# Optimization experiments

Measured on AMD Instinct MI355X. Metric: run time of the kernel, lower is better.

The kernel has to match this reference:

```python
import jax, jax.numpy as jnp
import numpy as np

D = 2048          # n_embd
H = 4 * D         # hidden_size
B, S = 4, 2048


def _make_masks(seed=0):
    rng = np.random.default_rng(seed)
    # mask1: for each group of 4 output rows, keep 2 of 4 rows (whole rows)
    mask1 = np.zeros((H, D), dtype=np.float32)
    for i in range(0, H, 4):
        keep = rng.permutation(4)[:2] + i
        mask1[keep, :] = 1.0
    # mask2: for each group of 4 input columns, keep 2 of 4 columns
    mask2 = np.zeros((D, H), dtype=np.float32)
    for i in range(0, H, 4):
        keep = rng.permutation(4)[:2] + i
        mask2[:, keep] = 1.0
    return jnp.asarray(mask1), jnp.asarray(mask2)


def setup_inputs() -> dict:
    key = jax.random.key(0)
    k_x, k_w1, k_w2 = jax.random.split(key, 3)
    x = jax.random.normal(k_x, (B, S, D), dtype=jnp.float32)
    # Kaiming-uniform-ish init like nn.Linear defaults
    w1 = jax.random.uniform(k_w1, (H, D), dtype=jnp.float32, minval=-1.0, maxval=1.0) / np.sqrt(D)
    w2 = jax.random.uniform(k_w2, (D, H), dtype=jnp.float32, minval=-1.0, maxval=1.0) / np.sqrt(H)
    mask1, mask2 = _make_masks()
    return {"x": x, "w1": w1, "w2": w2, "mask1": mask1, "mask2": mask2}


def reference(x, w1, w2, mask1, mask2):
    # sparse_multiply is elementwise mask application on the weights
    sw1 = w1 * mask1                      # [H, D]
    sw2 = w2 * mask2                      # [D, H]
    h = jnp.einsum('bsd,hd->bsh', x, sw1) # F.linear(x, sw1)
    h = jax.nn.gelu(h, approximate=False) # torch F.gelu default = exact erf
    out = jnp.einsum('bsh,dh->bsd', h, sw2)
    return out
```

## Files before the change

### kernel.cpp

```cpp
#include <hip/hip_runtime.h>
#include <hip/hip_bf16.h>

typedef __bf16 bf16_t;
typedef __bf16 bf16x8 __attribute__((ext_vector_type(8)));
typedef float f32x4 __attribute__((ext_vector_type(4)));

__device__ __forceinline__ unsigned short f32_to_bf16_rn(float f) {
  unsigned u = __float_as_uint(f);
  u += 0x7fffu + ((u >> 16) & 1u);
  return (unsigned short)(u >> 16);
}

__device__ __forceinline__ float gelu_exact(float x) {
  return 0.5f * x * (1.0f + erff(x * 0.7071067811865475f));
}

#define GLDS16(g, l)                                                          \
  __builtin_amdgcn_global_load_lds(                                           \
      (const __attribute__((address_space(1))) void*)(g),                     \
      (__attribute__((address_space(3))) void*)(l), 16, 0, 0)

__global__ void cast_x_kernel(const float* __restrict__ in,
                              unsigned short* __restrict__ out, int n4) {
  int i = blockIdx.x * blockDim.x + threadIdx.x;
  if (i >= n4) return;
  float4 v = ((const float4*)in)[i];
  ushort4 o;
  o.x = f32_to_bf16_rn(v.x);
  o.y = f32_to_bf16_rn(v.y);
  o.z = f32_to_bf16_rn(v.z);
  o.w = f32_to_bf16_rn(v.w);
  ((ushort4*)out)[i] = o;
}

__global__ void build_idx_kernel(const float* __restrict__ mask1,
                                 const float* __restrict__ mask2,
                                 int* __restrict__ idx, int* __restrict__ meta,
                                 int H, int D) {
  __shared__ int sums[1024];
  const int t = threadIdx.x;
  int flags[8];
  int tot = 0;
#pragma unroll
  for (int u = 0; u < 8; ++u) {
    int j = t * 8 + u;
    int f = (mask1[(long long)j * D] != 0.0f) && (mask2[j] != 0.0f);
    flags[u] = f;
    tot += f;
  }
  sums[t] = tot;
  __syncthreads();
  for (int off = 1; off < 1024; off <<= 1) {
    int v = (t >= off) ? sums[t - off] : 0;
    __syncthreads();
    sums[t] += v;
    __syncthreads();
  }
  int pos = sums[t] - tot;
#pragma unroll
  for (int u = 0; u < 8; ++u) {
    if (flags[u]) idx[pos++] = t * 8 + u;
  }
  if (t == 1023) {
    int count = sums[1023];
    meta[0] = count;
    meta[1] = (count + 127) & ~127;
  }
}

__global__ void compact_w1_kernel(const float* __restrict__ w1,
                                  const int* __restrict__ idx,
                                  const int* __restrict__ meta,
                                  unsigned short* __restrict__ w1c, int D) {
  int q = blockIdx.x * blockDim.x + threadIdx.x;
  int k = q >> 9;
  int d4 = (q & 511) << 2;
  int count = meta[0];
  ushort4 o = {0, 0, 0, 0};
  if (k < count) {
    int j = idx[k];
    float4 v = *(const float4*)(w1 + (long long)j * D + d4);
    o.x = f32_to_bf16_rn(v.x);
    o.y = f32_to_bf16_rn(v.y);
    o.z = f32_to_bf16_rn(v.z);
    o.w = f32_to_bf16_rn(v.w);
  }
  *(ushort4*)(w1c + (long long)k * D + d4) = o;
}

__global__ void compact_w2_kernel(const float* __restrict__ w2,
                                  const int* __restrict__ idx,
                                  const int* __restrict__ meta,
                                  unsigned short* __restrict__ w2c, int H) {
  int q = blockIdx.x * blockDim.x + threadIdx.x;
  int n = q >> 10;
  int k4 = (q & 1023) << 2;
  int count = meta[0];
  ushort4 o = {0, 0, 0, 0};
  const float* src = w2 + (long long)n * H;
#pragma unroll
  for (int u = 0; u < 4; ++u) {
    int k = k4 + u;
    unsigned short v = 0;
    if (k < count) v = f32_to_bf16_rn(src[idx[k]]);
    ((unsigned short*)&o)[u] = v;
  }
  *(ushort4*)(w2c + (long long)n * 4096 + k4) = o;
}

template <int EPI>
__global__ __launch_bounds__(256, 4) void gemm_pool_kernel(
    const bf16_t* __restrict__ A, const bf16_t* __restrict__ B,
    void* __restrict__ Cout, long long ldA, long long ldB, long long ldC,
    int Kfix, int ncolFix, const int* __restrict__ meta) {
  const int kpad = meta[1];
  const int K = (EPI == 0) ? kpad : Kfix;
  const int ncol = (EPI == 1) ? (kpad >> 6) : ncolFix;
  const int ntiles = ncol << 6;

  __shared__ bf16_t As[128 * 64];
  __shared__ bf16_t Bs[64 * 64];

  const int tid = threadIdx.x;
  const int l = tid & 63;
  const int w = tid >> 6;
  const int wm = w >> 1;
  const int wn = w & 1;

  const int srow = tid >> 3;
  const int sg = ((tid & 7) ^ ((tid >> 3) & 7)) * 8;

  const int fr = l & 15;
  const int gA = (l >> 4) ^ (l & 7);

  for (int tau = blockIdx.x; tau < ntiles; tau += gridDim.x) {
    const int row = tau & 63;
    const int col = tau >> 6;
    const long long brow = (long long)row * 128;
    const long long bcol = (long long)col * 64;

    const bf16_t* Ag = A + (brow + srow) * ldA + sg;
    const bf16_t* Bg = B + (bcol + srow) * ldB + sg;

    f32x4 acc[4][2];
#pragma unroll
    for (int m = 0; m < 4; ++m)
#pragma unroll
      for (int n = 0; n < 2; ++n) acc[m][n] = (f32x4){0.f, 0.f, 0.f, 0.f};

    for (int k0 = 0; k0 < K; k0 += 64) {
      GLDS16(Ag + k0, &As[tid * 8]);
      GLDS16(Ag + 32 * ldA + k0, &As[2048 + tid * 8]);
      GLDS16(Ag + 64 * ldA + k0, &As[4096 + tid * 8]);
      GLDS16(Ag + 96 * ldA + k0, &As[6144 + tid * 8]);
      GLDS16(Bg + k0, &Bs[tid * 8]);
      GLDS16(Bg + 32 * ldB + k0, &Bs[2048 + tid * 8]);
      __syncthreads();
#pragma unroll
      for (int kk = 0; kk < 2; ++kk) {
        const int gp = (gA ^ (kk * 4)) * 8;
        bf16x8 af[4], bfr[2];
#pragma unroll
        for (int m = 0; m < 4; ++m)
          af[m] = *(const bf16x8*)(&As[(wm * 64 + m * 16 + fr) * 64 + gp]);
#pragma unroll
        for (int n = 0; n < 2; ++n)
          bfr[n] = *(const bf16x8*)(&Bs[(wn * 32 + n * 16 + fr) * 64 + gp]);
#pragma unroll
        for (int m = 0; m < 4; ++m)
#pragma unroll
          for (int n = 0; n < 2; ++n)
            acc[m][n] = __builtin_amdgcn_mfma_f32_16x16x32_bf16(
                af[m], bfr[n], acc[m][n], 0, 0, 0);
      }
      __syncthreads();
    }

    const int orow = wm * 64 + (l >> 4) * 4;
    const int ocol = wn * 32 + fr;
#pragma unroll
    for (int m = 0; m < 4; ++m)
#pragma unroll
      for (int n = 0; n < 2; ++n)
#pragma unroll
        for (int r = 0; r < 4; ++r) {
          long long rr = brow + orow + m * 16 + r;
          long long cc = bcol + ocol + n * 16;
          float v = acc[m][n][r];
          if (EPI == 1) {
            ((unsigned short*)Cout)[rr * ldC + cc] =
                f32_to_bf16_rn(gelu_exact(v));
          } else {
            ((float*)Cout)[rr * ldC + cc] = v;
          }
        }
  }
}

extern "C" void kernel_launch(void* const* d_in, const int* in_sizes, int n_in,
                              void* d_out, int out_size, void* d_ws,
                              size_t ws_size, hipStream_t stream) {
  const float* x = (const float*)d_in[0];
  const float* w1 = (const float*)d_in[1];
  const float* w2 = (const float*)d_in[2];
  const float* mask1 = (const float*)d_in[3];
  const float* mask2 = (const float*)d_in[4];
  float* out = (float*)d_out;

  const int D = 2048, H = 8192, M = 8192;
  const int KP = 4096;

  char* ws = (char*)d_ws;
  unsigned short* xb = (unsigned short*)ws;
  unsigned short* w1c = xb + (size_t)M * D;
  unsigned short* w2c = w1c + (size_t)KP * D;
  unsigned short* hb = w2c + (size_t)D * KP;
  int* idx = (int*)(hb + (size_t)M * KP);
  int* meta = idx + KP;

  build_idx_kernel<<<1, 1024, 0, stream>>>(mask1, mask2, idx, meta, H, D);

  {
    int n4 = (M * D) / 4;
    cast_x_kernel<<<n4 / 256, 256, 0, stream>>>(x, xb, n4);
  }
  {
    int nq = KP * (D / 4);
    compact_w1_kernel<<<nq / 256, 256, 0, stream>>>(w1, idx, meta, w1c, D);
  }
  {
    int nq = D * (KP / 4);
    compact_w2_kernel<<<nq / 256, 256, 0, stream>>>(w2, idx, meta, w2c, H);
  }

  const int POOL = 2048;

  gemm_pool_kernel<1><<<POOL, 256, 0, stream>>>(
      (const bf16_t*)xb, (const bf16_t*)w1c, hb, (long long)D, (long long)D,
      (long long)KP, D, 0, meta);

  gemm_pool_kernel<0><<<POOL, 256, 0, stream>>>(
      (const bf16_t*)hb, (const bf16_t*)w2c, out, (long long)KP,
      (long long)KP, (long long)D, 0, 32, meta);
}
```

Before: 267.0 us.

## Fuse prep kernels, overlap w2 compaction with GEMM1, deepen K tile to 128

The x cast and w1 compaction are merged into one grid-stride prep kernel. The w2 compaction now runs on extra blocks appended to the first GEMM launch, so it overlaps with GEMM1 instead of being a separate serial launch. The GEMM K-step is doubled to 128, which doubles LDS per block and halves the number of barriers per tile. The larger LDS footprint lowers occupancy (launch bounds go from 4 to 3 blocks), and the appended w2 blocks compete with GEMM blocks for compute units.

New measurement: 272.3 us. No clear change (+2.0%).

```diff
diff --git a/kernel.cpp b/kernel.cpp
--- a/kernel.cpp
+++ b/kernel.cpp
@@ -11,27 +11,23 @@
   return (unsigned short)(u >> 16);
 }
 
-__device__ __forceinline__ float gelu_exact(float x) {
-  return 0.5f * x * (1.0f + erff(x * 0.7071067811865475f));
-}
-
-#define GLDS16(g, l)                                                          \
-  __builtin_amdgcn_global_load_lds(                                           \
-      (const __attribute__((address_space(1))) void*)(g),                     \
-      (__attribute__((address_space(3))) void*)(l), 16, 0, 0)
-
-__global__ void cast_x_kernel(const float* __restrict__ in,
-                              unsigned short* __restrict__ out, int n4) {
-  int i = blockIdx.x * blockDim.x + threadIdx.x;
-  if (i >= n4) return;
-  float4 v = ((const float4*)in)[i];
+__device__ __forceinline__ ushort4 cvt4(float4 v) {
   ushort4 o;
   o.x = f32_to_bf16_rn(v.x);
   o.y = f32_to_bf16_rn(v.y);
   o.z = f32_to_bf16_rn(v.z);
   o.w = f32_to_bf16_rn(v.w);
-  ((ushort4*)out)[i] = o;
-}
+  return o;
+}
+
+__device__ __forceinline__ float gelu_exact(float x) {
+  return 0.5f * x * (1.0f + erff(x * 0.7071067811865475f));
+}
+
+#define GLDS16(g, l)                                                          \
+  __builtin_amdgcn_global_load_lds(                                           \
+      (const __attribute__((address_space(1))) void*)(g),                     \
+      (__attribute__((address_space(3))) void*)(l), 16, 0, 0)
 
 __global__ void build_idx_kernel(const float* __restrict__ mask1,
                                  const float* __restrict__ mask2,
@@ -68,58 +64,68 @@
   }
 }
 
-__global__ void compact_w1_kernel(const float* __restrict__ w1,
-                                  const int* __restrict__ idx,
-                                  const int* __restrict__ meta,
-                                  unsigned short* __restrict__ w1c, int D) {
-  int q = blockIdx.x * blockDim.x + threadIdx.x;
-  int k = q >> 9;
-  int d4 = (q & 511) << 2;
-  int count = meta[0];
-  ushort4 o = {0, 0, 0, 0};
-  if (k < count) {
-    int j = idx[k];
-    float4 v = *(const float4*)(w1 + (long long)j * D + d4);
-    o.x = f32_to_bf16_rn(v.x);
-    o.y = f32_to_bf16_rn(v.y);
-    o.z = f32_to_bf16_rn(v.z);
-    o.w = f32_to_bf16_rn(v.w);
-  }
-  *(ushort4*)(w1c + (long long)k * D + d4) = o;
-}
-
-__global__ void compact_w2_kernel(const float* __restrict__ w2,
-                                  const int* __restrict__ idx,
-                                  const int* __restrict__ meta,
-                                  unsigned short* __restrict__ w2c, int H) {
-  int q = blockIdx.x * blockDim.x + threadIdx.x;
-  int n = q >> 10;
-  int k4 = (q & 1023) << 2;
-  int count = meta[0];
-  ushort4 o = {0, 0, 0, 0};
-  const float* src = w2 + (long long)n * H;
-#pragma unroll
-  for (int u = 0; u < 4; ++u) {
-    int k = k4 + u;
-    unsigned short v = 0;
-    if (k < count) v = f32_to_bf16_rn(src[idx[k]]);
-    ((unsigned short*)&o)[u] = v;
-  }
-  *(ushort4*)(w2c + (long long)n * 4096 + k4) = o;
-}
-
-template <int EPI>
-__global__ __launch_bounds__(256, 4) void gemm_pool_kernel(
+__global__ void prep_kernel(const float* __restrict__ x,
+                            const float* __restrict__ w1,
+                            const int* __restrict__ idx,
+                            const int* __restrict__ meta,
+                            unsigned short* __restrict__ xb,
+                            unsigned short* __restrict__ w1c, int D) {
+  const int nx = 4194304;
+  const int nw1 = 2097152;
+  const int count = meta[0];
+  for (int i = blockIdx.x * 256 + threadIdx.x; i < nx + nw1; i += 2048 * 256) {
+    if (i < nx) {
+      ((ushort4*)xb)[i] = cvt4(((const float4*)x)[i]);
+    } else {
+      int q = i - nx;
+      int k = q >> 9;
+      int d4 = (q & 511) << 2;
+      ushort4 o = {0, 0, 0, 0};
+      if (k < count)
+        o = cvt4(*(const float4*)(w1 + (long long)idx[k] * D + d4));
+      *(ushort4*)(w1c + (long long)k * D + d4) = o;
+    }
+  }
+}
+
+#define POOLG 2048
+#define W2BLKS 512
+
+template <int EPI, int DOW2>
+__global__ __launch_bounds__(256, 3) void gemm_pool_kernel(
     const bf16_t* __restrict__ A, const bf16_t* __restrict__ B,
     void* __restrict__ Cout, long long ldA, long long ldB, long long ldC,
-    int Kfix, int ncolFix, const int* __restrict__ meta) {
+    int Kfix, int ncolFix, const int* __restrict__ meta,
+    const float* __restrict__ w2src, const int* __restrict__ idx,
+    unsigned short* __restrict__ w2c, int H) {
+  if (DOW2 && blockIdx.x >= POOLG) {
+    const int nq = 2097152;
+    const int count = meta[0];
+    for (int q = (blockIdx.x - POOLG) * 256 + threadIdx.x; q < nq;
+         q += W2BLKS * 256) {
+      int n = q >> 10;
+      int k4 = (q & 1023) << 2;
+      ushort4 o = {0, 0, 0, 0};
+      const float* src = w2src + (long long)n * H;
+#pragma unroll
+      for (int u = 0; u < 4; ++u) {
+        int k = k4 + u;
+        unsigned short v = 0;
+        if (k < count) v = f32_to_bf16_rn(src[idx[k]]);
+        ((unsigned short*)&o)[u] = v;
+      }
+      *(ushort4*)(w2c + (long long)n * 4096 + k4) = o;
+    }
+    return;
+  }
+
   const int kpad = meta[1];
   const int K = (EPI == 0) ? kpad : Kfix;
   const int ncol = (EPI == 1) ? (kpad >> 6) : ncolFix;
   const int ntiles = ncol << 6;
 
-  __shared__ bf16_t As[128 * 64];
-  __shared__ bf16_t Bs[64 * 64];
+  __shared__ bf16_t As[128 * 128];
+  __shared__ bf16_t Bs[64 * 128];
 
   const int tid = threadIdx.x;
   const int l = tid & 63;
@@ -127,20 +133,19 @@
   const int wm = w >> 1;
   const int wn = w & 1;
 
-  const int srow = tid >> 3;
-  const int sg = ((tid & 7) ^ ((tid >> 3) & 7)) * 8;
+  const int srow = tid >> 4;
+  const int sgl = ((tid & 15) ^ ((tid >> 4) & 7)) * 8;
 
   const int fr = l & 15;
-  const int gA = (l >> 4) ^ (l & 7);
-
-  for (int tau = blockIdx.x; tau < ntiles; tau += gridDim.x) {
+
+  for (int tau = blockIdx.x; tau < ntiles; tau += POOLG) {
     const int row = tau & 63;
     const int col = tau >> 6;
     const long long brow = (long long)row * 128;
     const long long bcol = (long long)col * 64;
 
-    const bf16_t* Ag = A + (brow + srow) * ldA + sg;
-    const bf16_t* Bg = B + (bcol + srow) * ldB + sg;
+    const bf16_t* Ag = A + (brow + srow) * ldA + sgl;
+    const bf16_t* Bg = B + (bcol + srow) * ldB + sgl;
 
     f32x4 acc[4][2];
 #pragma unroll
@@ -148,24 +153,24 @@
 #pragma unroll
       for (int n = 0; n < 2; ++n) acc[m][n] = (f32x4){0.f, 0.f, 0.f, 0.f};
 
-    for (int k0 = 0; k0 < K; k0 += 64) {
-      GLDS16(Ag + k0, &As[tid * 8]);
-      GLDS16(Ag + 32 * ldA + k0, &As[2048 + tid * 8]);
-      GLDS16(Ag + 64 * ldA + k0, &As[4096 + tid * 8]);
-      GLDS16(Ag + 96 * ldA + k0, &As[6144 + tid * 8]);
-      GLDS16(Bg + k0, &Bs[tid * 8]);
-      GLDS16(Bg + 32 * ldB + k0, &Bs[2048 + tid * 8]);
+    for (int k0 = 0; k0 < K; k0 += 128) {
+#pragma unroll
+      for (int a = 0; a < 8; ++a)
+        GLDS16(Ag + a * 16 * ldA + k0, &As[a * 2048 + tid * 8]);
+#pragma unroll
+      for (int b = 0; b < 4; ++b)
+        GLDS16(Bg + b * 16 * ldB + k0, &Bs[b * 2048 + tid * 8]);
       __syncthreads();
 #pragma unroll
-      for (int kk = 0; kk < 2; ++kk) {
-        const int gp = (gA ^ (kk * 4)) * 8;
+      for (int kk = 0; kk < 4; ++kk) {
+        const int gp = ((((l >> 4) + 4 * kk) ^ (l & 7)) * 8);
         bf16x8 af[4], bfr[2];
 #pragma unroll
         for (int m = 0; m < 4; ++m)
-          af[m] = *(const bf16x8*)(&As[(wm * 64 + m * 16 + fr) * 64 + gp]);
+          af[m] = *(const bf16x8*)(&As[(wm * 64 + m * 16 + fr) * 128 + gp]);
 #pragma unroll
         for (int n = 0; n < 2; ++n)
-          bfr[n] = *(const bf16x8*)(&Bs[(wn * 32 + n * 16 + fr) * 64 + gp]);
+          bfr[n] = *(const bf16x8*)(&Bs[(wn * 32 + n * 16 + fr) * 128 + gp]);
 #pragma unroll
         for (int m = 0; m < 4; ++m)
 #pragma unroll
@@ -220,26 +225,13 @@
 
   build_idx_kernel<<<1, 1024, 0, stream>>>(mask1, mask2, idx, meta, H, D);
 
-  {
-    int n4 = (M * D) / 4;
-    cast_x_kernel<<<n4 / 256, 256, 0, stream>>>(x, xb, n4);
-  }
-  {
-    int nq = KP * (D / 4);
-    compact_w1_kernel<<<nq / 256, 256, 0, stream>>>(w1, idx, meta, w1c, D);
-  }
-  {
-    int nq = D * (KP / 4);
-    compact_w2_kernel<<<nq / 256, 256, 0, stream>>>(w2, idx, meta, w2c, H);
-  }
-
-  const int POOL = 2048;
-
-  gemm_pool_kernel<1><<<POOL, 256, 0, stream>>>(
+  prep_kernel<<<2048, 256, 0, stream>>>(x, w1, idx, meta, xb, w1c, D);
+
+  gemm_pool_kernel<1, 1><<<POOLG + W2BLKS, 256, 0, stream>>>(
       (const bf16_t*)xb, (const bf16_t*)w1c, hb, (long long)D, (long long)D,
-      (long long)KP, D, 0, meta);
-
-  gemm_pool_kernel<0><<<POOL, 256, 0, stream>>>(
+      (long long)KP, D, 0, meta, w2, idx, w2c, H);
+
+  gemm_pool_kernel<0, 0><<<POOLG, 256, 0, stream>>>(
       (const bf16_t*)hb, (const bf16_t*)w2c, out, (long long)KP,
-      (long long)KP, (long long)D, 0, 32, meta);
-}
+      (long long)KP, (long long)D, 0, 32, meta, nullptr, nullptr, nullptr, H);
+}
```
